# Kernel optimization log

Measured on AMD Instinct MI355X. Metric: run time of the kernel, lower is better.

## Reference

```python
import math
import jax, jax.numpy as jnp
import numpy as np

B, S, HID, H, NREL = 4, 512, 1024, 16, 64
D = HID // H  # per-head size = 64, must equal relation embedding dim


def setup_inputs() -> dict:
    key = jax.random.key(0)
    ks = jax.random.split(key, 12)
    w = lambda k, shape: jax.random.normal(k, shape, jnp.float32) * 0.02
    return {
        "q_in": jax.random.normal(ks[0], (B, S, HID), jnp.float32),
        "k_in": jax.random.normal(ks[1], (B, S, HID), jnp.float32),
        "v_in": jax.random.normal(ks[2], (B, S, HID), jnp.float32),
        "mask": jax.random.randint(ks[3], (B, 1, S, S), 0, NREL),
        "Wq": w(ks[4], (HID, HID)), "bq": jnp.zeros((HID,), jnp.float32),
        "Wk": w(ks[5], (HID, HID)), "bk": jnp.zeros((HID,), jnp.float32),
        "Wv": w(ks[6], (HID, HID)), "bv": jnp.zeros((HID,), jnp.float32),
        "Wo": w(ks[7], (HID, HID)), "bo": jnp.zeros((HID,), jnp.float32),
        "rel_k_table": w(ks[8], (NREL, D)),
        "rel_v_table": w(ks[9], (NREL, D)),
    }


def reference(q_in, k_in, v_in, mask, Wq, bq, Wk, bk, Wv, bv, Wo, bo,
              rel_k_table, rel_v_table):
    def proj(x, W, b):  # [B,S,HID] -> [B,H,S,D]
        return (x @ W.T + b).reshape(B, S, H, D).transpose(0, 2, 1, 3)

    q = proj(q_in, Wq, bq)
    k = proj(k_in, Wk, bk)
    v = proj(v_in, Wv, bv)

    ids = mask[:, 0]                      # [B,S,S] relation ids
    rel_k = rel_k_table[ids]              # [B,S,S,D]
    rel_v = rel_v_table[ids]              # [B,S,S,D]

    scores = jnp.einsum('bhqd,bhkd->bhqk', q, k)
    scores = scores + jnp.einsum('bhqd,bqkd->bhqk', q, rel_k) / 4.0
    scores = scores / math.sqrt(float(D))

    bias = (1.0 - (mask > 0).astype(scores.dtype)) * -10000.0  # [B,1,S,S]
    probs = jax.nn.softmax(scores + bias, axis=-1)             # [B,H,S,S]

    out = jnp.einsum('bhqk,bhkd->bhqd', probs, v)
    out = out + 0.25 * jnp.einsum('bhqk,bqkd->bhqd', probs, rel_v)
    out = out.transpose(0, 2, 1, 3).reshape(B, S, HID)
    return out @ Wo.T + bo
```

## Files before the change

### kernel.cpp

```cpp
#include <hip/hip_runtime.h>


typedef __attribute__((ext_vector_type(8))) short bf16x8 __attribute__((may_alias));
typedef __attribute__((ext_vector_type(4))) float f32x4;

__device__ __forceinline__ short f2bf(float x) {
    unsigned u = __float_as_uint(x);
    u += 0x7fff + ((u >> 16) & 1);
    return (short)(u >> 16);
}

__device__ __forceinline__ void async16(void* lds, const void* g) {
    __builtin_amdgcn_global_load_lds(
        (const __attribute__((address_space(1))) void*)g,
        (__attribute__((address_space(3))) void*)lds, 16, 0, 0);
}

__global__ __launch_bounds__(256)
void cast_all(const float* __restrict__ x0, const float* __restrict__ x1, const float* __restrict__ x2,
              const float* __restrict__ w0, const float* __restrict__ w1,
              const float* __restrict__ w2, const float* __restrict__ w3,
              const float* __restrict__ rk, const float* __restrict__ rv,
              short* __restrict__ y0, short* __restrict__ y1, short* __restrict__ y2,
              short* __restrict__ u0, short* __restrict__ u1,
              short* __restrict__ u2, short* __restrict__ u3,
              short* __restrict__ rkb, short* __restrict__ rvT)
{
    size_t i = (size_t)blockIdx.x * 256 + threadIdx.x;
    if (i < 2621440u) {
        const float* src; short* dst; size_t off;
        if (i < 3u*524288u) {
            int s = (int)(i / 524288u); off = i % 524288u;
            src = s == 0 ? x0 : (s == 1 ? x1 : x2);
            dst = s == 0 ? y0 : (s == 1 ? y1 : y2);
        } else {
            size_t j = i - 3u*524288u;
            int s = (int)(j / 262144u); off = j % 262144u;
            src = s == 0 ? w0 : (s == 1 ? w1 : (s == 2 ? w2 : w3));
            dst = s == 0 ? u0 : (s == 1 ? u1 : (s == 2 ? u2 : u3));
        }
        float4 f = ((const float4*)src)[off];
        short4 o; o.x = f2bf(f.x); o.y = f2bf(f.y); o.z = f2bf(f.z); o.w = f2bf(f.w);
        ((short4*)dst)[off] = o;
    } else if (i < 2621440u + 1024u) {
        size_t off = i - 2621440u;
        float4 f = ((const float4*)rk)[off];
        short4 o; o.x = f2bf(f.x); o.y = f2bf(f.y); o.z = f2bf(f.z); o.w = f2bf(f.w);
        ((short4*)rkb)[off] = o;
    } else {
        int m = (int)(i - 2622464u);
        int d = m >> 4, r0 = (m & 15) * 4;
        short4 o;
        o.x = f2bf(rv[(size_t)(r0 + 0) * 64 + d]);
        o.y = f2bf(rv[(size_t)(r0 + 1) * 64 + d]);
        o.z = f2bf(rv[(size_t)(r0 + 2) * 64 + d]);
        o.w = f2bf(rv[(size_t)(r0 + 3) * 64 + d]);
        *(short4*)&rvT[d * 64 + r0] = o;
    }
}

__global__ __launch_bounds__(256)
void gemm12864(const short* __restrict__ A0, const short* __restrict__ A1, const short* __restrict__ A2,
               const short* __restrict__ B0, const short* __restrict__ B1, const short* __restrict__ B2,
               const float* __restrict__ c0, const float* __restrict__ c1, const float* __restrict__ c2,
               void* __restrict__ O0, void* __restrict__ O1, void* __restrict__ O2,
               int mode)
{
    __shared__ short ldsw[2 * 12288];

    const int z = blockIdx.z;
    const short* A    = z == 0 ? A0 : (z == 1 ? A1 : A2);
    const short* Bm   = z == 0 ? B0 : (z == 1 ? B1 : B2);
    const float* bias = z == 0 ? c0 : (z == 1 ? c1 : c2);
    void*        O    = z == 0 ? O0 : (z == 1 ? O1 : O2);

    const int t = threadIdx.x;
    const int lane = t & 63, w = t >> 6;
    const int wr = w >> 1, wc = w & 1;
    const int quad = lane >> 4, cl = lane & 15;
    const int rowBase = blockIdx.y * 128;
    const int colBase = blockIdx.x * 64;
    const int gl = ((lane & 7) - (lane >> 3)) & 7;

    f32x4 acc[4][2];
#pragma unroll
    for (int i = 0; i < 4; ++i)
#pragma unroll
        for (int j = 0; j < 2; ++j) acc[i][j] = (f32x4){0.f, 0.f, 0.f, 0.f};

    const int rstage = w * 8 + (lane >> 3);
    const short* Ag = A  + (size_t)(rowBase + rstage) * 1024 + gl * 8;
    const short* Bg = Bm + (size_t)(colBase + rstage) * 1024 + gl * 8;

    {
        short* Als = ldsw;
        short* Bls = ldsw + 8192;
#pragma unroll
        for (int i = 0; i < 4; ++i)
            async16(&Als[(i * 32 + w * 8) * 64], Ag + (size_t)i * 32 * 1024);
#pragma unroll
        for (int i = 0; i < 2; ++i)
            async16(&Bls[(i * 32 + w * 8) * 64], Bg + (size_t)i * 32 * 1024);
    }

    for (int it = 0; it < 16; ++it) {
        const int cur = it & 1;
        __syncthreads();
        if (it < 15) {
            short* Als = ldsw + (cur ^ 1) * 12288;
            short* Bls = Als + 8192;
            const int k0 = (it + 1) * 64;
#pragma unroll
            for (int i = 0; i < 4; ++i)
                async16(&Als[(i * 32 + w * 8) * 64], Ag + (size_t)i * 32 * 1024 + k0);
#pragma unroll
            for (int i = 0; i < 2; ++i)
                async16(&Bls[(i * 32 + w * 8) * 64], Bg + (size_t)i * 32 * 1024 + k0);
        }
        const short* Als = ldsw + cur * 12288;
        const short* Bls = Als + 8192;
#pragma unroll
        for (int kk = 0; kk < 2; ++kk) {
            bf16x8 a[4], b[2];
#pragma unroll
            for (int mi = 0; mi < 4; ++mi) {
                int r = wr * 64 + mi * 16 + cl;
                int s = (kk * 4 + quad + r) & 7;
                a[mi] = *(const bf16x8*)&Als[r * 64 + s * 8];
            }
#pragma unroll
            for (int ni = 0; ni < 2; ++ni) {
                int r = wc * 32 + ni * 16 + cl;
                int s = (kk * 4 + quad + r) & 7;
                b[ni] = *(const bf16x8*)&Bls[r * 64 + s * 8];
            }
#pragma unroll
            for (int mi = 0; mi < 4; ++mi)
#pragma unroll
                for (int ni = 0; ni < 2; ++ni)
                    acc[mi][ni] = __builtin_amdgcn_mfma_f32_16x16x32_bf16(
                        a[mi], b[ni], acc[mi][ni], 0, 0, 0);
        }
    }

    if (mode == 0) {
#pragma unroll
        for (int mi = 0; mi < 4; ++mi)
#pragma unroll
            for (int ni = 0; ni < 2; ++ni) {
                int col = colBase + wc * 32 + ni * 16 + cl;
                float bv = bias[col];
#pragma unroll
                for (int reg = 0; reg < 4; ++reg) {
                    int row = rowBase + wr * 64 + mi * 16 + quad * 4 + reg;
                    ((float*)O)[(size_t)row * 1024 + col] = acc[mi][ni][reg] + bv;
                }
            }
        return;
    }

    __syncthreads();
    short* Tls = ldsw;
    if (z == 2) {
#pragma unroll
        for (int mi = 0; mi < 4; ++mi)
#pragma unroll
            for (int ni = 0; ni < 2; ++ni) {
                int d = wc * 32 + ni * 16 + cl;
                float bv = bias[colBase + d];
                short4 pk;
                pk.x = f2bf(acc[mi][ni][0] + bv);
                pk.y = f2bf(acc[mi][ni][1] + bv);
                pk.z = f2bf(acc[mi][ni][2] + bv);
                pk.w = f2bf(acc[mi][ni][3] + bv);
                int sl = wr * 64 + mi * 16 + quad * 4;
                *(short4*)&Tls[d * 136 + sl] = pk;
            }
        __syncthreads();
        int d = t >> 2, s0 = (t & 3) * 32;
        int bb = rowBase >> 9, sBase = rowBase & 511, hh = colBase >> 6;
        short* dst = (short*)O + (((size_t)(bb * 16 + hh) * 64 + d) << 9) + sBase + s0;
#pragma unroll
        for (int j = 0; j < 4; ++j)
            *(bf16x8*)(dst + j * 8) = *(const bf16x8*)&Tls[d * 136 + s0 + j * 8];
    } else {
#pragma unroll
        for (int mi = 0; mi < 4; ++mi)
#pragma unroll
            for (int ni = 0; ni < 2; ++ni) {
                int d = wc * 32 + ni * 16 + cl;
                float bv = bias[colBase + d];
#pragma unroll
                for (int reg = 0; reg < 4; ++reg) {
                    int sl = wr * 64 + mi * 16 + quad * 4 + reg;
                    Tls[sl * 72 + d] = f2bf(acc[mi][ni][reg] + bv);
                }
            }
        __syncthreads();
        int sl = t >> 1, half = t & 1;
        int bb = rowBase >> 9, sBase = rowBase & 511, hh = colBase >> 6;
        short* dst = (short*)O + (((size_t)(bb * 16 + hh) * 512 + sBase + sl) << 6) + half * 32;
#pragma unroll
        for (int j = 0; j < 4; ++j)
            *(bf16x8*)(dst + j * 8) = *(const bf16x8*)&Tls[sl * 72 + half * 32 + j * 8];
    }
}

#define AT_BINS 4352
#define AT_PST  8704
#define AT_TOT  11264

__global__ __launch_bounds__(64, 2)
void attn_kernel(const short* __restrict__ qg, const short* __restrict__ kg,
                 const short* __restrict__ vtg, const int* __restrict__ mask,
                 const short* __restrict__ relkb, const short* __restrict__ relvT,
                 short* __restrict__ attn_b)
{
    __shared__ __align__(16) char pool[AT_TOT];
    float* qwr    = (float*)pool;
    float* bins   = (float*)(pool + AT_BINS);
    short* Pst    = (short*)(pool + AT_PST);
    short* binsBf = Pst;

    const int lane = threadIdx.x;
    const int quad = lane >> 4, cl = lane & 15;
    const int bid = blockIdx.x;
    const int bh = bid & 63, qbk = bid >> 6;
    const int b = bh >> 4, h = bh & 15, q0 = qbk * 16;

    const short* qbase = qg  + ((size_t)bh * 512 + q0) * 64;
    const short* kbase = kg  + (size_t)bh * 512 * 64;
    const short* vbase = vtg + (size_t)bh * 64 * 512;
    const int*   mb    = mask + (size_t)b * 512 * 512 + (size_t)q0 * 512;

    for (int i = lane; i < 16 * 68; i += 64) bins[i] = 0.f;

    bf16x8 qa0 = *(const bf16x8*)(qbase + cl * 64 + quad * 8);
    bf16x8 qa1 = *(const bf16x8*)(qbase + cl * 64 + 32 + quad * 8);

    bf16x8 kbuf[2][8];
    int    idb[2][16];
#pragma unroll
    for (int nt = 0; nt < 4; ++nt) {
        const short* kp = kbase + (size_t)(nt * 16 + cl) * 64 + quad * 8;
        kbuf[0][nt * 2]     = *(const bf16x8*)kp;
        kbuf[0][nt * 2 + 1] = *(const bf16x8*)(kp + 32);
    }
#pragma unroll
    for (int nt = 0; nt < 4; ++nt)
#pragma unroll
        for (int reg = 0; reg < 4; ++reg)
            idb[0][nt * 4 + reg] = mb[(size_t)(quad * 4 + reg) * 512 + nt * 16 + cl];

#pragma unroll
    for (int rt = 0; rt < 4; ++rt) {
        const short* kp = relkb + (size_t)(rt * 16 + cl) * 64 + quad * 8;
        bf16x8 rb0 = *(const bf16x8*)kp;
        bf16x8 rb1 = *(const bf16x8*)(kp + 32);
        f32x4 qr = (f32x4){0.f, 0.f, 0.f, 0.f};
        qr = __builtin_amdgcn_mfma_f32_16x16x32_bf16(qa0, rb0, qr, 0, 0, 0);
        qr = __builtin_amdgcn_mfma_f32_16x16x32_bf16(qa1, rb1, qr, 0, 0, 0);
#pragma unroll
        for (int reg = 0; reg < 4; ++reg)
            qwr[(quad * 4 + reg) * 68 + rt * 16 + cl] = qr[reg];
    }

    f32x4 oacc[4];
#pragma unroll
    for (int dt = 0; dt < 4; ++dt) oacc[dt] = (f32x4){0.f, 0.f, 0.f, 0.f};
    float lpart[4] = {0.f, 0.f, 0.f, 0.f};

#pragma unroll
    for (int c = 0; c < 8; ++c) {
        const int cur = c & 1, nxt = cur ^ 1;
        const int k0 = c * 64;

        float qv[16];
#pragma unroll
        for (int e = 0; e < 16; ++e)
            qv[e] = qwr[(quad * 4 + (e & 3)) * 68 + idb[cur][e]];

        bf16x8 vb[8];
#pragma unroll
        for (int dt = 0; dt < 4; ++dt) {
            const short* vp = vbase + (size_t)(dt * 16 + cl) * 512 + k0 + quad * 8;
            vb[dt * 2]     = *(const bf16x8*)vp;
            vb[dt * 2 + 1] = *(const bf16x8*)(vp + 32);
        }

        if (c < 7) {
            const int k1 = k0 + 64;
#pragma unroll
            for (int nt = 0; nt < 4; ++nt) {
                const short* kp = kbase + (size_t)(k1 + nt * 16 + cl) * 64 + quad * 8;
                kbuf[nxt][nt * 2]     = *(const bf16x8*)kp;
                kbuf[nxt][nt * 2 + 1] = *(const bf16x8*)(kp + 32);
            }
#pragma unroll
            for (int nt = 0; nt < 4; ++nt)
#pragma unroll
                for (int reg = 0; reg < 4; ++reg)
                    idb[nxt][nt * 4 + reg] = mb[(size_t)(quad * 4 + reg) * 512 + k1 + nt * 16 + cl];
        }

#pragma unroll
        for (int nt = 0; nt < 4; ++nt) {
            f32x4 s = (f32x4){0.f, 0.f, 0.f, 0.f};
            s = __builtin_amdgcn_mfma_f32_16x16x32_bf16(qa0, kbuf[cur][nt * 2],     s, 0, 0, 0);
            s = __builtin_amdgcn_mfma_f32_16x16x32_bf16(qa1, kbuf[cur][nt * 2 + 1], s, 0, 0, 0);
#pragma unroll
            for (int reg = 0; reg < 4; ++reg) {
                int q = quad * 4 + reg;
                int id = idb[cur][nt * 4 + reg];
                float sc = fmaf(qv[nt * 4 + reg], 0.03125f, s[reg] * 0.125f);
                float p = (id == 0) ? 0.f : __expf(sc);
                lpart[reg] += p;
                atomicAdd(&bins[q * 68 + id], p);
                Pst[q * 72 + nt * 16 + cl] = f2bf(p);
            }
        }
        bf16x8 pa0 = *(const bf16x8*)&Pst[cl * 72 + quad * 8];
        bf16x8 pa1 = *(const bf16x8*)&Pst[cl * 72 + 32 + quad * 8];
#pragma unroll
        for (int dt = 0; dt < 4; ++dt) {
            oacc[dt] = __builtin_amdgcn_mfma_f32_16x16x32_bf16(pa0, vb[dt * 2],     oacc[dt], 0, 0, 0);
            oacc[dt] = __builtin_amdgcn_mfma_f32_16x16x32_bf16(pa1, vb[dt * 2 + 1], oacc[dt], 0, 0, 0);
        }
    }

    float invq[4];
#pragma unroll
    for (int reg = 0; reg < 4; ++reg) {
        float l = lpart[reg];
#pragma unroll
        for (int m = 8; m >= 1; m >>= 1) l += __shfl_xor(l, m);
        invq[reg] = 1.0f / l;
    }

    {
        int q = lane >> 2, r0 = (lane & 3) * 16;
#pragma unroll
        for (int j = 0; j < 4; ++j) {
            float4 f = *(const float4*)&bins[q * 68 + r0 + j * 4];
            short4 o;
            o.x = f2bf(f.x); o.y = f2bf(f.y); o.z = f2bf(f.z); o.w = f2bf(f.w);
            *(short4*)&binsBf[q * 72 + r0 + j * 4] = o;
        }
    }

    bf16x8 ba0 = *(const bf16x8*)&binsBf[cl * 72 + quad * 8];
    bf16x8 ba1 = *(const bf16x8*)&binsBf[cl * 72 + 32 + quad * 8];
#pragma unroll
    for (int dt = 0; dt < 4; ++dt) {
        const short* rp = relvT + (size_t)(dt * 16 + cl) * 64 + quad * 8;
        bf16x8 rv0 = *(const bf16x8*)rp;
        bf16x8 rv1 = *(const bf16x8*)(rp + 32);
        f32x4 racc = (f32x4){0.f, 0.f, 0.f, 0.f};
        racc = __builtin_amdgcn_mfma_f32_16x16x32_bf16(ba0, rv0, racc, 0, 0, 0);
        racc = __builtin_amdgcn_mfma_f32_16x16x32_bf16(ba1, rv1, racc, 0, 0, 0);
#pragma unroll
        for (int reg = 0; reg < 4; ++reg) {
            int q = quad * 4 + reg;
            float val = (oacc[dt][reg] + 0.25f * racc[reg]) * invq[reg];
            attn_b[(size_t)(b * 512 + q0 + q) * 1024 + h * 64 + dt * 16 + cl] = f2bf(val);
        }
    }
}

extern "C" void kernel_launch(void* const* d_in, const int* in_sizes, int n_in,
                              void* d_out, int out_size, void* d_ws, size_t ws_size,
                              hipStream_t stream)
{
    const float* q_in = (const float*)d_in[0];
    const float* k_in = (const float*)d_in[1];
    const float* v_in = (const float*)d_in[2];
    const int*   mask = (const int*)d_in[3];
    const float* Wq   = (const float*)d_in[4];
    const float* bq   = (const float*)d_in[5];
    const float* Wk   = (const float*)d_in[6];
    const float* bk   = (const float*)d_in[7];
    const float* Wv   = (const float*)d_in[8];
    const float* bv   = (const float*)d_in[9];
    const float* Wo   = (const float*)d_in[10];
    const float* bo   = (const float*)d_in[11];
    const float* relk = (const float*)d_in[12];
    const float* relv = (const float*)d_in[13];

    char* ws = (char*)d_ws;
    short* qb     = (short*)(ws);
    short* kb     = (short*)(ws + (4u  << 20));
    short* vt     = (short*)(ws + (8u  << 20));
    short* attn_b = (short*)(ws + (12u << 20));
    short* Xq     = (short*)(ws + (16u << 20));
    short* Xk     = (short*)(ws + (20u << 20));
    short* Xv     = (short*)(ws + (24u << 20));
    short* Wqb    = (short*)(ws + (28u << 20));
    short* Wkb    = (short*)(ws + (30u << 20));
    short* Wvb    = (short*)(ws + (32u << 20));
    short* Wob    = (short*)(ws + (34u << 20));
    short* relkb  = (short*)(ws + (36u << 20));
    short* relvT  = (short*)(ws + (36u << 20) + 8192);

    cast_all<<<10248, 256, 0, stream>>>(q_in, k_in, v_in, Wq, Wk, Wv, Wo, relk, relv,
                                        Xq, Xk, Xv, Wqb, Wkb, Wvb, Wob, relkb, relvT);

    gemm12864<<<dim3(16, 16, 3), 256, 0, stream>>>(
        Xq, Xk, Xv, Wqb, Wkb, Wvb, bq, bk, bv, qb, kb, vt, 1);

    attn_kernel<<<dim3(2048), 64, 0, stream>>>(qb, kb, vt, mask, relkb, relvT, attn_b);

    gemm12864<<<dim3(16, 16, 1), 256, 0, stream>>>(
        attn_b, attn_b, attn_b, Wob, Wob, Wob, bo, bo, bo,
        (void*)d_out, (void*)d_out, (void*)d_out, 0);
}
```

Measured before the change: 245.9 us.

## Compress mask to uint8, pack four attention waves per block, drop register prefetch

The int32 relation-id mask is converted to uint8 in the cast kernel, so attention reads a quarter of the mask bytes. The attention kernel now runs four independent 64-lane waves per 256-thread block, each with its own LDS slice, covering 64 query rows per block. The K/id double-buffered register prefetch and the full unroll of the chunk loop are removed, with loads issued inline to lower register pressure. s_setprio is raised around the MFMA groups. This trades explicit latency hiding for occupancy and adds a mask conversion pass to the cast kernel.

Result: faster. 236.4 us (-3.8%).

```diff
diff --git a/kernel.cpp b/kernel.cpp
--- a/kernel.cpp
+++ b/kernel.cpp
@@ -21,10 +21,12 @@
               const float* __restrict__ w0, const float* __restrict__ w1,
               const float* __restrict__ w2, const float* __restrict__ w3,
               const float* __restrict__ rk, const float* __restrict__ rv,
+              const int* __restrict__ mask,
               short* __restrict__ y0, short* __restrict__ y1, short* __restrict__ y2,
               short* __restrict__ u0, short* __restrict__ u1,
               short* __restrict__ u2, short* __restrict__ u3,
-              short* __restrict__ rkb, short* __restrict__ rvT)
+              short* __restrict__ rkb, short* __restrict__ rvT,
+              unsigned char* __restrict__ mu8)
 {
     size_t i = (size_t)blockIdx.x * 256 + threadIdx.x;
     if (i < 2621440u) {
@@ -47,7 +49,7 @@
         float4 f = ((const float4*)rk)[off];
         short4 o; o.x = f2bf(f.x); o.y = f2bf(f.y); o.z = f2bf(f.z); o.w = f2bf(f.w);
         ((short4*)rkb)[off] = o;
-    } else {
+    } else if (i < 2622464u + 1024u) {
         int m = (int)(i - 2622464u);
         int d = m >> 4, r0 = (m & 15) * 4;
         short4 o;
@@ -56,6 +58,13 @@
         o.z = f2bf(rv[(size_t)(r0 + 2) * 64 + d]);
         o.w = f2bf(rv[(size_t)(r0 + 3) * 64 + d]);
         *(short4*)&rvT[d * 64 + r0] = o;
+    } else if (i < 2623488u + 262144u) {
+        size_t m = i - 2623488u;
+        int4 v = ((const int4*)mask)[m];
+        uchar4 o;
+        o.x = (unsigned char)v.x; o.y = (unsigned char)v.y;
+        o.z = (unsigned char)v.z; o.w = (unsigned char)v.w;
+        ((uchar4*)mu8)[m] = o;
     }
 }
 
@@ -208,49 +217,37 @@
 
 #define AT_BINS 4352
 #define AT_PST  8704
-#define AT_TOT  11264
-
-__global__ __launch_bounds__(64, 2)
+#define AT_SLICE 11264
+
+__global__ __launch_bounds__(256)
 void attn_kernel(const short* __restrict__ qg, const short* __restrict__ kg,
-                 const short* __restrict__ vtg, const int* __restrict__ mask,
+                 const short* __restrict__ vtg, const unsigned char* __restrict__ mu8,
                  const short* __restrict__ relkb, const short* __restrict__ relvT,
                  short* __restrict__ attn_b)
 {
-    __shared__ __align__(16) char pool[AT_TOT];
-    float* qwr    = (float*)pool;
-    float* bins   = (float*)(pool + AT_BINS);
-    short* Pst    = (short*)(pool + AT_PST);
+    __shared__ __align__(16) char pool[4 * AT_SLICE];
+    const int t = threadIdx.x;
+    const int lane = t & 63, w = t >> 6;
+    char* mypool = pool + w * AT_SLICE;
+    float* qwr    = (float*)mypool;
+    float* bins   = (float*)(mypool + AT_BINS);
+    short* Pst    = (short*)(mypool + AT_PST);
     short* binsBf = Pst;
 
-    const int lane = threadIdx.x;
     const int quad = lane >> 4, cl = lane & 15;
     const int bid = blockIdx.x;
-    const int bh = bid & 63, qbk = bid >> 6;
-    const int b = bh >> 4, h = bh & 15, q0 = qbk * 16;
+    const int bh = bid & 63, qq = bid >> 6;
+    const int b = bh >> 4, h = bh & 15, q0 = qq * 64 + w * 16;
 
     const short* qbase = qg  + ((size_t)bh * 512 + q0) * 64;
     const short* kbase = kg  + (size_t)bh * 512 * 64;
     const short* vbase = vtg + (size_t)bh * 64 * 512;
-    const int*   mb    = mask + (size_t)b * 512 * 512 + (size_t)q0 * 512;
+    const unsigned char* mb = mu8 + (size_t)b * 512 * 512 + (size_t)q0 * 512;
 
     for (int i = lane; i < 16 * 68; i += 64) bins[i] = 0.f;
 
     bf16x8 qa0 = *(const bf16x8*)(qbase + cl * 64 + quad * 8);
     bf16x8 qa1 = *(const bf16x8*)(qbase + cl * 64 + 32 + quad * 8);
-
-    bf16x8 kbuf[2][8];
-    int    idb[2][16];
-#pragma unroll
-    for (int nt = 0; nt < 4; ++nt) {
-        const short* kp = kbase + (size_t)(nt * 16 + cl) * 64 + quad * 8;
-        kbuf[0][nt * 2]     = *(const bf16x8*)kp;
-        kbuf[0][nt * 2 + 1] = *(const bf16x8*)(kp + 32);
-    }
-#pragma unroll
-    for (int nt = 0; nt < 4; ++nt)
-#pragma unroll
-        for (int reg = 0; reg < 4; ++reg)
-            idb[0][nt * 4 + reg] = mb[(size_t)(quad * 4 + reg) * 512 + nt * 16 + cl];
 
 #pragma unroll
     for (int rt = 0; rt < 4; ++rt) {
@@ -270,15 +267,14 @@
     for (int dt = 0; dt < 4; ++dt) oacc[dt] = (f32x4){0.f, 0.f, 0.f, 0.f};
     float lpart[4] = {0.f, 0.f, 0.f, 0.f};
 
-#pragma unroll
     for (int c = 0; c < 8; ++c) {
-        const int cur = c & 1, nxt = cur ^ 1;
         const int k0 = c * 64;
-
-        float qv[16];
-#pragma unroll
-        for (int e = 0; e < 16; ++e)
-            qv[e] = qwr[(quad * 4 + (e & 3)) * 68 + idb[cur][e]];
+        int ids[4][4];
+#pragma unroll
+        for (int nt = 0; nt < 4; ++nt)
+#pragma unroll
+            for (int reg = 0; reg < 4; ++reg)
+                ids[nt][reg] = mb[(size_t)(quad * 4 + reg) * 512 + k0 + nt * 16 + cl];
 
         bf16x8 vb[8];
 #pragma unroll
@@ -288,31 +284,22 @@
             vb[dt * 2 + 1] = *(const bf16x8*)(vp + 32);
         }
 
-        if (c < 7) {
-            const int k1 = k0 + 64;
-#pragma unroll
-            for (int nt = 0; nt < 4; ++nt) {
-                const short* kp = kbase + (size_t)(k1 + nt * 16 + cl) * 64 + quad * 8;
-                kbuf[nxt][nt * 2]     = *(const bf16x8*)kp;
-                kbuf[nxt][nt * 2 + 1] = *(const bf16x8*)(kp + 32);
-            }
-#pragma unroll
-            for (int nt = 0; nt < 4; ++nt)
-#pragma unroll
-                for (int reg = 0; reg < 4; ++reg)
-                    idb[nxt][nt * 4 + reg] = mb[(size_t)(quad * 4 + reg) * 512 + k1 + nt * 16 + cl];
-        }
-
 #pragma unroll
         for (int nt = 0; nt < 4; ++nt) {
+            const int kidx = k0 + nt * 16 + cl;
+            const short* kp = kbase + (size_t)kidx * 64 + quad * 8;
+            bf16x8 kb0 = *(const bf16x8*)kp;
+            bf16x8 kb1 = *(const bf16x8*)(kp + 32);
             f32x4 s = (f32x4){0.f, 0.f, 0.f, 0.f};
-            s = __builtin_amdgcn_mfma_f32_16x16x32_bf16(qa0, kbuf[cur][nt * 2],     s, 0, 0, 0);
-            s = __builtin_amdgcn_mfma_f32_16x16x32_bf16(qa1, kbuf[cur][nt * 2 + 1], s, 0, 0, 0);
+            __builtin_amdgcn_s_setprio(1);
+            s = __builtin_amdgcn_mfma_f32_16x16x32_bf16(qa0, kb0, s, 0, 0, 0);
+            s = __builtin_amdgcn_mfma_f32_16x16x32_bf16(qa1, kb1, s, 0, 0, 0);
+            __builtin_amdgcn_s_setprio(0);
 #pragma unroll
             for (int reg = 0; reg < 4; ++reg) {
                 int q = quad * 4 + reg;
-                int id = idb[cur][nt * 4 + reg];
-                float sc = fmaf(qv[nt * 4 + reg], 0.03125f, s[reg] * 0.125f);
+                int id = ids[nt][reg];
+                float sc = (s[reg] + 0.25f * qwr[q * 68 + id]) * 0.125f;
                 float p = (id == 0) ? 0.f : __expf(sc);
                 lpart[reg] += p;
                 atomicAdd(&bins[q * 68 + id], p);
@@ -321,11 +308,13 @@
         }
         bf16x8 pa0 = *(const bf16x8*)&Pst[cl * 72 + quad * 8];
         bf16x8 pa1 = *(const bf16x8*)&Pst[cl * 72 + 32 + quad * 8];
+        __builtin_amdgcn_s_setprio(1);
 #pragma unroll
         for (int dt = 0; dt < 4; ++dt) {
             oacc[dt] = __builtin_amdgcn_mfma_f32_16x16x32_bf16(pa0, vb[dt * 2],     oacc[dt], 0, 0, 0);
             oacc[dt] = __builtin_amdgcn_mfma_f32_16x16x32_bf16(pa1, vb[dt * 2 + 1], oacc[dt], 0, 0, 0);
         }
+        __builtin_amdgcn_s_setprio(0);
     }
 
     float invq[4];
@@ -400,14 +389,15 @@
     short* Wob    = (short*)(ws + (34u << 20));
     short* relkb  = (short*)(ws + (36u << 20));
     short* relvT  = (short*)(ws + (36u << 20) + 8192);
-
-    cast_all<<<10248, 256, 0, stream>>>(q_in, k_in, v_in, Wq, Wk, Wv, Wo, relk, relv,
-                                        Xq, Xk, Xv, Wqb, Wkb, Wvb, Wob, relkb, relvT);
+    unsigned char* masku8 = (unsigned char*)(ws + (36u << 20) + 16384);
+
+    cast_all<<<11272, 256, 0, stream>>>(q_in, k_in, v_in, Wq, Wk, Wv, Wo, relk, relv, mask,
+                                        Xq, Xk, Xv, Wqb, Wkb, Wvb, Wob, relkb, relvT, masku8);
 
     gemm12864<<<dim3(16, 16, 3), 256, 0, stream>>>(
         Xq, Xk, Xv, Wqb, Wkb, Wvb, bq, bk, bv, qb, kb, vt, 1);
 
-    attn_kernel<<<dim3(2048), 64, 0, stream>>>(qb, kb, vt, mask, relkb, relvT, attn_b);
+    attn_kernel<<<dim3(512), 256, 0, stream>>>(qb, kb, vt, masku8, relkb, relvT, attn_b);
 
     gemm12864<<<dim3(16, 16, 1), 256, 0, stream>>>(
         attn_b, attn_b, attn_b, Wob, Wob, Wob, bo, bo, bo,
```
